# Optimization experiments

Measured on AMD Instinct MI355X. Metric: run time of the kernel, lower is better.

## Reference

```python
import jax, jax.numpy as jnp
import numpy as np

BETA = 0.25
ALPHA = 1.0
K, D = 1024, 256
B, H, W = 16, 64, 64

def setup_inputs() -> dict:
    key = jax.random.key(0)
    k1, k2 = jax.random.split(key)
    latents = jax.random.normal(k1, (B, D, H, W), dtype=jnp.float32)
    # nn.Embedding init: uniform(-1/K, 1/K)
    embedding_weight = jax.random.uniform(k2, (K, D), dtype=jnp.float32,
                                          minval=-1.0 / K, maxval=1.0 / K)
    return {"latents": latents, "embedding_weight": embedding_weight}

def reference(latents, embedding_weight):
    # NCHW -> NHWC, flatten to [N, D]
    lat = jnp.transpose(latents, (0, 2, 3, 1))            # [B,H,W,D]
    flat = lat.reshape(-1, D)                             # [N,D]
    dist = (jnp.sum(flat * flat, axis=1, keepdims=True)
            + jnp.sum(embedding_weight * embedding_weight, axis=1)
            - 2.0 * flat @ embedding_weight.T)            # [N,K]
    inds = jnp.argmin(dist, axis=1)                        # [N]
    quant = embedding_weight[inds].reshape(lat.shape)      # [B,H,W,D] (gather == one-hot matmul)
    embedding_loss = jnp.mean((quant - jax.lax.stop_gradient(lat)) ** 2)
    commitment_loss = jnp.mean((jax.lax.stop_gradient(quant) - lat) ** 2)
    vq_loss = commitment_loss * BETA + embedding_loss * ALPHA
    # straight-through estimator
    out = lat + jax.lax.stop_gradient(quant - lat)
    out = jnp.transpose(out, (0, 3, 1, 2))                 # back to NCHW
    return out, vq_loss, inds.reshape(B, H, W)
```

## Files before the change

### kernel.cpp

```cpp
#include <hip/hip_runtime.h>
#include <math.h>

#define KCODES 1024
#define DDIM 256
#define NHW 4096
#define NROWS 65536
#define NELEM 16777216
#define LOSS_OFF NELEM
#define INDS_OFF (NELEM + 1)

#define WS_LOSS 0
#define WS_COUNT 8
#define WS_LIST 16
#define WS_BV   262160
#define WS_BPP  266256

#define DELTA 2e-4f

using bf16x8 = __attribute__((ext_vector_type(8))) short;
using f32x4  = __attribute__((ext_vector_type(4))) float;

static __device__ __forceinline__ unsigned short f2bf(float f) {
  unsigned int u = __float_as_uint(f);
  u += 0x7fffu + ((u >> 16) & 1u);
  return (unsigned short)(u >> 16);
}
static __device__ __forceinline__ float bf2f(unsigned short h) {
  return __uint_as_float(((unsigned int)h) << 16);
}

__global__ __launch_bounds__(256) void prep_kernel(const float* __restrict__ emb,
                                                   unsigned short* __restrict__ Bpp,
                                                   float* __restrict__ Bv,
                                                   int* __restrict__ count,
                                                   double* __restrict__ loss_acc) {
#pragma clang fp contract(off)
  if (blockIdx.x < 256) {
    const int i = blockIdx.x * 256 + threadIdx.x;
    const int l = i & 63;
    const int kb = (i >> 6) & 15;
    const int g = i >> 10;
    const int code = g * 16 + (l & 15);
    const int kp0 = kb * 32 + (l >> 4) * 8;
    const int hi_half = (kp0 < 256);
    const int d0 = hi_half ? kp0 : (kp0 - 256);
    const float* ep = emb + (size_t)code * DDIM + d0;
    unsigned short v[8];
#pragma unroll
    for (int j = 0; j < 8; ++j) {
      float x = ep[j];
      unsigned short h = f2bf(x);
      if (hi_half) v[j] = h;
      else v[j] = f2bf(x - bf2f(h));
    }
    unsigned short* dst = Bpp + ((size_t)(g * 16 + kb) * 64 + l) * 8;
#pragma unroll
    for (int j = 0; j < 8; ++j) dst[j] = v[j];
  } else {
    if (blockIdx.x == 259 && threadIdx.x == 0) {
      *count = 0;
      *loss_acc = 0.0;
    }
    const int k = (blockIdx.x - 256) * 256 + threadIdx.x;
    const float* p = emb + (size_t)k * DDIM;
    float half[2];
    for (int h = 0; h < 2; ++h) {
      float r[8];
#pragma unroll
      for (int j = 0; j < 8; ++j) {
        float v = p[h * 128 + j];
        r[j] = v * v;
      }
      for (int i = 8; i < 128; i += 8) {
#pragma unroll
        for (int j = 0; j < 8; ++j) {
          float v = p[h * 128 + i + j];
          r[j] += v * v;
        }
      }
      half[h] = ((r[0] + r[1]) + (r[2] + r[3])) + ((r[4] + r[5]) + (r[6] + r[7]));
    }
    Bv[k] = half[0] + half[1];
  }
}

__global__ __launch_bounds__(1024) void screen_kernel(
    const float* __restrict__ lat, const unsigned short* __restrict__ Bpp,
    const float* __restrict__ Bv, float* __restrict__ inds_f,
    int* __restrict__ list, int* __restrict__ count,
    double* __restrict__ loss_acc) {
  __shared__ __align__(16) char AsF[64 * 1024];
  __shared__ float BvS[KCODES];
  __shared__ float Xsq[16][64];
  __shared__ float Mg1[64][9];
  __shared__ float Mg2[64][9];
  __shared__ int   Mgi[64][9];

  const int tid = threadIdx.x;
  const int n0 = blockIdx.x * 64;
  const int b = n0 >> 12;
  const int hw0 = n0 & 4095;

  BvS[tid] = Bv[tid];

  {
    const int m = tid & 63;
    const int mr = m >> 4, lr15 = m & 15;
    const int db0 = tid >> 6;
    const float* base = lat + (size_t)b * (DDIM * NHW) + hw0 + m;
    float sq = 0.f;
#pragma unroll
    for (int t = 0; t < 2; ++t) {
      const int db = db0 + t * 16;
      const int d0 = db * 8;
      const int tch = db >> 2;
      const int q = db & 3;
      bf16x8 hv, lv;
#pragma unroll
      for (int j = 0; j < 8; ++j) {
        float x = __builtin_nontemporal_load(&base[(size_t)(d0 + j) * NHW]);
        sq += x * x;
        unsigned short h = f2bf(x);
        hv[j] = (short)h;
        lv[j] = (short)f2bf(x - bf2f(h));
      }
      const int slot = (q * 16 + lr15) * 16;
      *(bf16x8*)(AsF + (size_t)(tch * 4 + mr) * 1024 + slot) = hv;
      *(bf16x8*)(AsF + (size_t)((8 + tch) * 4 + mr) * 1024 + slot) = lv;
    }
    Xsq[db0][m] = sq;
  }
  __syncthreads();

  const int w = tid >> 6;
  const int l = tid & 63;
  const int mhalf = w & 1;
  const int nslice = w >> 1;
  const int lr = l & 15;
  const int lk = l >> 4;

  f32x4 acc[2][8];
#pragma unroll
  for (int mr = 0; mr < 2; ++mr)
#pragma unroll
    for (int nr = 0; nr < 8; ++nr)
      acc[mr][nr] = (f32x4){0.f, 0.f, 0.f, 0.f};

  const unsigned short* Bl = Bpp + (size_t)l * 8;
  const char* AsL = AsF + l * 16;

  for (int t = 0; t < 8; ++t) {
    bf16x8 afh[2], afl[2];
#pragma unroll
    for (int mr = 0; mr < 2; ++mr) {
      const int gmr = mhalf * 2 + mr;
      afh[mr] = *(const bf16x8*)(AsL + (size_t)(t * 4 + gmr) * 1024);
      afl[mr] = *(const bf16x8*)(AsL + (size_t)((8 + t) * 4 + gmr) * 1024);
    }
#pragma unroll
    for (int nr = 0; nr < 8; ++nr) {
      const int g = nslice * 8 + nr;
      bf16x8 bh = *(const bf16x8*)(Bl + (size_t)(g * 16 + t) * 512);
      bf16x8 bl = *(const bf16x8*)(Bl + (size_t)(g * 16 + 8 + t) * 512);
      acc[0][nr] = __builtin_amdgcn_mfma_f32_16x16x32_bf16(afh[0], bh, acc[0][nr], 0, 0, 0);
      acc[1][nr] = __builtin_amdgcn_mfma_f32_16x16x32_bf16(afh[1], bh, acc[1][nr], 0, 0, 0);
      acc[0][nr] = __builtin_amdgcn_mfma_f32_16x16x32_bf16(afl[0], bh, acc[0][nr], 0, 0, 0);
      acc[1][nr] = __builtin_amdgcn_mfma_f32_16x16x32_bf16(afl[1], bh, acc[1][nr], 0, 0, 0);
      acc[0][nr] = __builtin_amdgcn_mfma_f32_16x16x32_bf16(afh[0], bl, acc[0][nr], 0, 0, 0);
      acc[1][nr] = __builtin_amdgcn_mfma_f32_16x16x32_bf16(afh[1], bl, acc[1][nr], 0, 0, 0);
    }
  }

#pragma unroll
  for (int mr = 0; mr < 2; ++mr) {
#pragma unroll
    for (int j = 0; j < 4; ++j) {
      float m1 = 1e30f, m2 = 1e30f;
      int i1 = 1 << 30;
#pragma unroll
      for (int nr = 0; nr < 8; ++nr) {
        const int c = nslice * 128 + nr * 16 + lr;
        const float s = BvS[c] - 2.0f * acc[mr][nr][j];
        if (s < m1) { m2 = m1; m1 = s; i1 = c; }
        else if (s < m2) m2 = s;
      }
#pragma unroll
      for (int off = 1; off < 16; off <<= 1) {
        float o1 = __shfl_xor(m1, off, 16);
        float o2 = __shfl_xor(m2, off, 16);
        int oi = __shfl_xor(i1, off, 16);
        if (o1 < m1 || (o1 == m1 && oi < i1)) {
          m2 = fminf(m1, o2);
          m1 = o1; i1 = oi;
        } else {
          m2 = fminf(m2, o1);
        }
      }
      if (lr == 0) {
        const int row = mhalf * 32 + mr * 16 + lk * 4 + j;
        Mg1[row][nslice] = m1;
        Mg2[row][nslice] = m2;
        Mgi[row][nslice] = i1;
      }
    }
  }
  __syncthreads();

  if (tid < 64) {
    float g1 = 1e30f, g2 = 1e30f;
    int gi = 1 << 30;
#pragma unroll
    for (int sl = 0; sl < 8; ++sl) {
      const float m1 = Mg1[tid][sl], m2 = Mg2[tid][sl];
      const int ii = Mgi[tid][sl];
      if (m1 < g1 || (m1 == g1 && ii < gi)) {
        g2 = fminf(g1, m2);
        g1 = m1; gi = ii;
      } else {
        g2 = fminf(g2, m1);
      }
    }
    const int n = n0 + tid;
    inds_f[n] = (float)gi;
    if (g2 - g1 < DELTA) {
      int p = atomicAdd(count, 1);
      list[p] = n;
    }
    float x2 = 0.f;
#pragma unroll
    for (int k = 0; k < 16; ++k) x2 += Xsq[k][tid];
    float rowloss = x2 + g1;
    for (int off = 32; off > 0; off >>= 1)
      rowloss += __shfl_down(rowloss, off, 64);
    if (tid == 0) atomicAdd(loss_acc, (double)rowloss);
  }
}

__global__ __launch_bounds__(256) void refine_kernel(
    const float* __restrict__ lat, const float* __restrict__ emb,
    const float* __restrict__ Bv, float* __restrict__ inds_f,
    const int* __restrict__ list, const int* __restrict__ count) {
#pragma clang fp contract(off)
  __shared__ float xs[8][DDIM];
  __shared__ float rjs[8][2][8];
  __shared__ float Asm[8];
  __shared__ float rsv[4][8];
  __shared__ int rsi[4][8];
  const int cnt = *count;
  const int tid = threadIdx.x;
  for (int base = blockIdx.x * 8; base < cnt; base += gridDim.x * 8) {
    const int nr = min(8, cnt - base);
    for (int r = 0; r < nr; ++r) {
      const int n = list[base + r];
      const int bb = n >> 12, hw = n & 4095;
      xs[r][tid] = lat[((size_t)(bb * DDIM + tid)) * NHW + hw];
    }
    __syncthreads();

    if (tid < 128) {
      const int r = tid >> 4, h = (tid >> 3) & 1, j = tid & 7;
      const float* xr = &xs[r][h * 128 + j];
      float v = xr[0];
      float acc = v * v;
      for (int s = 1; s < 16; ++s) { v = xr[s * 8]; acc += v * v; }
      rjs[r][h][j] = acc;
    }
    __syncthreads();
    if (tid < 8) {
      const float* q0 = rjs[tid][0];
      const float* q1 = rjs[tid][1];
      float h0 = ((q0[0] + q0[1]) + (q0[2] + q0[3])) + ((q0[4] + q0[5]) + (q0[6] + q0[7]));
      float h1 = ((q1[0] + q1[1]) + (q1[2] + q1[3])) + ((q1[4] + q1[5]) + (q1[6] + q1[7]));
      Asm[tid] = h0 + h1;
    }
    __syncthreads();

    float best[8];
    int bidx[8];
#pragma unroll
    for (int r = 0; r < 8; ++r) { best[r] = 1e30f; bidx[r] = KCODES; }

    for (int c = 0; c < 4; ++c) {
      const int k = c * 256 + tid;
      const float4* e4 = (const float4*)(emb + (size_t)k * DDIM);
      float acc[8] = {0.f, 0.f, 0.f, 0.f, 0.f, 0.f, 0.f, 0.f};
      for (int d4 = 0; d4 < 64; ++d4) {
        const float4 e = e4[d4];
#pragma unroll
        for (int r = 0; r < 8; ++r) {
          acc[r] = __builtin_fmaf(xs[r][d4 * 4 + 0], e.x, acc[r]);
          acc[r] = __builtin_fmaf(xs[r][d4 * 4 + 1], e.y, acc[r]);
          acc[r] = __builtin_fmaf(xs[r][d4 * 4 + 2], e.z, acc[r]);
          acc[r] = __builtin_fmaf(xs[r][d4 * 4 + 3], e.w, acc[r]);
        }
      }
      const float bk = Bv[k];
#pragma unroll
      for (int r = 0; r < 8; ++r) {
        const float S = Asm[r] + bk;
        const float s = S - 2.0f * acc[r];
        if (s < best[r] || (s == best[r] && k < bidx[r])) { best[r] = s; bidx[r] = k; }
      }
    }

#pragma unroll
    for (int r = 0; r < 8; ++r) {
      float bv = best[r];
      int bi = bidx[r];
      for (int off = 32; off > 0; off >>= 1) {
        const float ov = __shfl_down(bv, off, 64);
        const int oi = __shfl_down(bi, off, 64);
        if (ov < bv || (ov == bv && oi < bi)) { bv = ov; bi = oi; }
      }
      const int lane = tid & 63, wid = tid >> 6;
      if (lane == 0) { rsv[wid][r] = bv; rsi[wid][r] = bi; }
    }
    __syncthreads();
    if (tid < 8 && tid < nr) {
      float bv = rsv[0][tid];
      int bi = rsi[0][tid];
      for (int ww = 1; ww < 4; ++ww) {
        const float ov = rsv[ww][tid];
        const int oi = rsi[ww][tid];
        if (ov < bv || (ov == bv && oi < bi)) { bv = ov; bi = oi; }
      }
      inds_f[list[base + tid]] = (float)bi;
    }
    __syncthreads();
  }
}

__global__ __launch_bounds__(256) void qwrite_kernel(
    const float* __restrict__ emb, const float* __restrict__ inds_f,
    const double* __restrict__ loss_acc, float* __restrict__ out) {
  __shared__ float Ls[256][65];
  const int tid = threadIdx.x;
  const int n0 = blockIdx.x * 64;
  const int b = n0 >> 12;
  const int hw0 = n0 & 4095;

  if (blockIdx.x == 0 && tid == 0) {
    double mse = *loss_acc / (double)NELEM;
    out[LOSS_OFF] = (float)(1.25 * mse);
  }

  {
    const int m = tid >> 2;
    const int q = tid & 3;
    const int ind = (int)inds_f[n0 + m];
    const float4* src = (const float4*)(emb + (size_t)ind * DDIM + q * 64);
#pragma unroll
    for (int jj = 0; jj < 16; ++jj) {
      const int j4 = (jj + q * 4) & 15;
      float4 v = src[j4];
      const int e = q * 64 + j4 * 4;
      Ls[e + 0][m] = v.x;
      Ls[e + 1][m] = v.y;
      Ls[e + 2][m] = v.z;
      Ls[e + 3][m] = v.w;
    }
  }
  __syncthreads();

  {
    const int m = tid & 63;
    const int wv = tid >> 6;
    float* obase = out + (size_t)b * (DDIM * NHW) + hw0 + m;
#pragma unroll
    for (int i = 0; i < 64; ++i) {
      const int d = i * 4 + wv;
      __builtin_nontemporal_store(Ls[d][m], &obase[(size_t)d * NHW]);
    }
  }
}

extern "C" void kernel_launch(void* const* d_in, const int* in_sizes, int n_in,
                              void* d_out, int out_size, void* d_ws, size_t ws_size,
                              hipStream_t stream) {
  const float* lat = (const float*)d_in[0];
  const float* emb = (const float*)d_in[1];
  float* out = (float*)d_out;
  char* ws = (char*)d_ws;
  double* loss_acc = (double*)(ws + WS_LOSS);
  int* count = (int*)(ws + WS_COUNT);
  int* list = (int*)(ws + WS_LIST);
  float* Bv = (float*)(ws + WS_BV);
  unsigned short* Bpp = (unsigned short*)(ws + WS_BPP);
  float* inds_f = out + INDS_OFF;

  hipLaunchKernelGGL(prep_kernel, dim3(260), dim3(256), 0, stream,
                     emb, Bpp, Bv, count, loss_acc);
  hipLaunchKernelGGL(screen_kernel, dim3(NROWS / 64), dim3(1024), 0, stream,
                     lat, Bpp, Bv, inds_f, list, count, loss_acc);
  hipLaunchKernelGGL(refine_kernel, dim3(4096), dim3(256), 0, stream,
                     lat, emb, Bv, inds_f, list, count);
  hipLaunchKernelGGL(qwrite_kernel, dim3(NROWS / 64), dim3(256), 0, stream,
                     emb, inds_f, loss_acc, out);
}
```

Measured before the change: 244.8 us.

## Switch screening GEMM to 32x32x16 MFMA tiles with repacked operands

Replaces the 16x16x32 bf16 MFMA tiling in the screen kernel with 32x32x16 MFMAs. The LDS activation layout and the global codebook packing are rearranged to match, and each wave now covers all 64 rows against 64 codes. The argmin reduction is reworked for the 32-wide output layout and merges 16 wave slices instead of 8. The larger MFMA shape is meant to raise operand reuse and cut fragment-load and instruction overhead. In exchange, reductions need more shuffle steps over the 16 accumulator registers.

```diff
diff --git a/kernel.cpp b/kernel.cpp
--- a/kernel.cpp
+++ b/kernel.cpp
@@ -18,7 +18,7 @@
 #define DELTA 2e-4f
 
 using bf16x8 = __attribute__((ext_vector_type(8))) short;
-using f32x4  = __attribute__((ext_vector_type(4))) float;
+using f32x16 = __attribute__((ext_vector_type(16))) float;
 
 static __device__ __forceinline__ unsigned short f2bf(float f) {
   unsigned int u = __float_as_uint(f);
@@ -38,22 +38,22 @@
   if (blockIdx.x < 256) {
     const int i = blockIdx.x * 256 + threadIdx.x;
     const int l = i & 63;
-    const int kb = (i >> 6) & 15;
-    const int g = i >> 10;
-    const int code = g * 16 + (l & 15);
-    const int kp0 = kb * 32 + (l >> 4) * 8;
-    const int hi_half = (kp0 < 256);
-    const int d0 = hi_half ? kp0 : (kp0 - 256);
+    const int cb = (i >> 6) & 31;
+    const int g32 = i >> 11;
+    const int code = g32 * 32 + (l & 31);
+    const int half = cb >> 4;
+    const int ks = cb & 15;
+    const int d0 = ks * 16 + (l >> 5) * 8;
     const float* ep = emb + (size_t)code * DDIM + d0;
     unsigned short v[8];
 #pragma unroll
     for (int j = 0; j < 8; ++j) {
       float x = ep[j];
       unsigned short h = f2bf(x);
-      if (hi_half) v[j] = h;
+      if (half == 0) v[j] = h;
       else v[j] = f2bf(x - bf2f(h));
     }
-    unsigned short* dst = Bpp + ((size_t)(g * 16 + kb) * 64 + l) * 8;
+    unsigned short* dst = Bpp + ((size_t)(g32 * 32 + cb) * 64 + l) * 8;
 #pragma unroll
     for (int j = 0; j < 8; ++j) dst[j] = v[j];
   } else {
@@ -92,9 +92,9 @@
   __shared__ __align__(16) char AsF[64 * 1024];
   __shared__ float BvS[KCODES];
   __shared__ float Xsq[16][64];
-  __shared__ float Mg1[64][9];
-  __shared__ float Mg2[64][9];
-  __shared__ int   Mgi[64][9];
+  __shared__ float Mg1[64][17];
+  __shared__ float Mg2[64][17];
+  __shared__ int   Mgi[64][17];
 
   const int tid = threadIdx.x;
   const int n0 = blockIdx.x * 64;
@@ -105,7 +105,8 @@
 
   {
     const int m = tid & 63;
-    const int mr = m >> 4, lr15 = m & 15;
+    const int rt = m >> 5;
+    const int m31 = m & 31;
     const int db0 = tid >> 6;
     const float* base = lat + (size_t)b * (DDIM * NHW) + hw0 + m;
     float sq = 0.f;
@@ -113,8 +114,8 @@
     for (int t = 0; t < 2; ++t) {
       const int db = db0 + t * 16;
       const int d0 = db * 8;
-      const int tch = db >> 2;
-      const int q = db & 3;
+      const int ks = db >> 1;
+      const int l5 = db & 1;
       bf16x8 hv, lv;
 #pragma unroll
       for (int j = 0; j < 8; ++j) {
@@ -124,9 +125,9 @@
         hv[j] = (short)h;
         lv[j] = (short)f2bf(x - bf2f(h));
       }
-      const int slot = (q * 16 + lr15) * 16;
-      *(bf16x8*)(AsF + (size_t)(tch * 4 + mr) * 1024 + slot) = hv;
-      *(bf16x8*)(AsF + (size_t)((8 + tch) * 4 + mr) * 1024 + slot) = lv;
+      const int slot = ((l5 << 5) | m31) * 16;
+      *(bf16x8*)(AsF + (size_t)(ks * 2 + rt) * 1024 + slot) = hv;
+      *(bf16x8*)(AsF + (size_t)(32 + ks * 2 + rt) * 1024 + slot) = lv;
     }
     Xsq[db0][m] = sq;
   }
@@ -134,61 +135,55 @@
 
   const int w = tid >> 6;
   const int l = tid & 63;
-  const int mhalf = w & 1;
-  const int nslice = w >> 1;
-  const int lr = l & 15;
-  const int lk = l >> 4;
-
-  f32x4 acc[2][8];
-#pragma unroll
-  for (int mr = 0; mr < 2; ++mr)
-#pragma unroll
-    for (int nr = 0; nr < 8; ++nr)
-      acc[mr][nr] = (f32x4){0.f, 0.f, 0.f, 0.f};
+
+  f32x16 acc[2][2];
+#pragma unroll
+  for (int rt = 0; rt < 2; ++rt)
+#pragma unroll
+    for (int ct = 0; ct < 2; ++ct)
+#pragma unroll
+      for (int e = 0; e < 16; ++e) acc[rt][ct][e] = 0.f;
 
   const unsigned short* Bl = Bpp + (size_t)l * 8;
   const char* AsL = AsF + l * 16;
 
-  for (int t = 0; t < 8; ++t) {
-    bf16x8 afh[2], afl[2];
-#pragma unroll
-    for (int mr = 0; mr < 2; ++mr) {
-      const int gmr = mhalf * 2 + mr;
-      afh[mr] = *(const bf16x8*)(AsL + (size_t)(t * 4 + gmr) * 1024);
-      afl[mr] = *(const bf16x8*)(AsL + (size_t)((8 + t) * 4 + gmr) * 1024);
-    }
-#pragma unroll
-    for (int nr = 0; nr < 8; ++nr) {
-      const int g = nslice * 8 + nr;
-      bf16x8 bh = *(const bf16x8*)(Bl + (size_t)(g * 16 + t) * 512);
-      bf16x8 bl = *(const bf16x8*)(Bl + (size_t)(g * 16 + 8 + t) * 512);
-      acc[0][nr] = __builtin_amdgcn_mfma_f32_16x16x32_bf16(afh[0], bh, acc[0][nr], 0, 0, 0);
-      acc[1][nr] = __builtin_amdgcn_mfma_f32_16x16x32_bf16(afh[1], bh, acc[1][nr], 0, 0, 0);
-      acc[0][nr] = __builtin_amdgcn_mfma_f32_16x16x32_bf16(afl[0], bh, acc[0][nr], 0, 0, 0);
-      acc[1][nr] = __builtin_amdgcn_mfma_f32_16x16x32_bf16(afl[1], bh, acc[1][nr], 0, 0, 0);
-      acc[0][nr] = __builtin_amdgcn_mfma_f32_16x16x32_bf16(afh[0], bl, acc[0][nr], 0, 0, 0);
-      acc[1][nr] = __builtin_amdgcn_mfma_f32_16x16x32_bf16(afh[1], bl, acc[1][nr], 0, 0, 0);
-    }
-  }
-
-#pragma unroll
-  for (int mr = 0; mr < 2; ++mr) {
-#pragma unroll
-    for (int j = 0; j < 4; ++j) {
-      float m1 = 1e30f, m2 = 1e30f;
-      int i1 = 1 << 30;
-#pragma unroll
-      for (int nr = 0; nr < 8; ++nr) {
-        const int c = nslice * 128 + nr * 16 + lr;
-        const float s = BvS[c] - 2.0f * acc[mr][nr][j];
-        if (s < m1) { m2 = m1; m1 = s; i1 = c; }
-        else if (s < m2) m2 = s;
-      }
-#pragma unroll
-      for (int off = 1; off < 16; off <<= 1) {
-        float o1 = __shfl_xor(m1, off, 16);
-        float o2 = __shfl_xor(m2, off, 16);
-        int oi = __shfl_xor(i1, off, 16);
+  for (int ks = 0; ks < 16; ++ks) {
+    bf16x8 ahi[2], alo[2];
+#pragma unroll
+    for (int rt = 0; rt < 2; ++rt) {
+      ahi[rt] = *(const bf16x8*)(AsL + (size_t)(ks * 2 + rt) * 1024);
+      alo[rt] = *(const bf16x8*)(AsL + (size_t)(32 + ks * 2 + rt) * 1024);
+    }
+#pragma unroll
+    for (int ct = 0; ct < 2; ++ct) {
+      const int g32 = w * 2 + ct;
+      bf16x8 bh = *(const bf16x8*)(Bl + (size_t)(g32 * 32 + ks) * 512);
+      bf16x8 bl_ = *(const bf16x8*)(Bl + (size_t)(g32 * 32 + 16 + ks) * 512);
+      acc[0][ct] = __builtin_amdgcn_mfma_f32_32x32x16_bf16(ahi[0], bh, acc[0][ct], 0, 0, 0);
+      acc[1][ct] = __builtin_amdgcn_mfma_f32_32x32x16_bf16(ahi[1], bh, acc[1][ct], 0, 0, 0);
+      acc[0][ct] = __builtin_amdgcn_mfma_f32_32x32x16_bf16(alo[0], bh, acc[0][ct], 0, 0, 0);
+      acc[1][ct] = __builtin_amdgcn_mfma_f32_32x32x16_bf16(alo[1], bh, acc[1][ct], 0, 0, 0);
+      acc[0][ct] = __builtin_amdgcn_mfma_f32_32x32x16_bf16(ahi[0], bl_, acc[0][ct], 0, 0, 0);
+      acc[1][ct] = __builtin_amdgcn_mfma_f32_32x32x16_bf16(ahi[1], bl_, acc[1][ct], 0, 0, 0);
+    }
+  }
+
+#pragma unroll
+  for (int rt = 0; rt < 2; ++rt) {
+#pragma unroll
+    for (int reg = 0; reg < 16; ++reg) {
+      const int c0 = w * 64 + (l & 31);
+      const float s0 = BvS[c0] - 2.0f * acc[rt][0][reg];
+      const float s1 = BvS[c0 + 32] - 2.0f * acc[rt][1][reg];
+      float m1, m2;
+      int i1;
+      if (s1 < s0) { m1 = s1; i1 = c0 + 32; m2 = s0; }
+      else { m1 = s0; i1 = c0; m2 = s1; }
+#pragma unroll
+      for (int off = 1; off < 32; off <<= 1) {
+        float o1 = __shfl_xor(m1, off, 32);
+        float o2 = __shfl_xor(m2, off, 32);
+        int oi = __shfl_xor(i1, off, 32);
         if (o1 < m1 || (o1 == m1 && oi < i1)) {
           m2 = fminf(m1, o2);
           m1 = o1; i1 = oi;
@@ -196,11 +191,11 @@
           m2 = fminf(m2, o1);
         }
       }
-      if (lr == 0) {
-        const int row = mhalf * 32 + mr * 16 + lk * 4 + j;
-        Mg1[row][nslice] = m1;
-        Mg2[row][nslice] = m2;
-        Mgi[row][nslice] = i1;
+      if ((l & 31) == 0) {
+        const int row = rt * 32 + (reg & 3) + 8 * (reg >> 2) + 4 * (l >> 5);
+        Mg1[row][w] = m1;
+        Mg2[row][w] = m2;
+        Mgi[row][w] = i1;
       }
     }
   }
@@ -210,7 +205,7 @@
     float g1 = 1e30f, g2 = 1e30f;
     int gi = 1 << 30;
 #pragma unroll
-    for (int sl = 0; sl < 8; ++sl) {
+    for (int sl = 0; sl < 16; ++sl) {
       const float m1 = Mg1[tid][sl], m2 = Mg2[tid][sl];
       const int ii = Mgi[tid][sl];
       if (m1 < g1 || (m1 == g1 && ii < gi)) {
```

Measured after the change: 314.3 us. 1.28x slower.
